# Optimization experiments

Measured on AMD Instinct MI355X. Metric: run time of the kernel, lower is better.

The kernel has to match this reference:

```python
import jax, jax.numpy as jnp
import numpy as np

KW = 4.0                     # kernel_width
P = int(np.ceil(KW) + 2)     # taps per axis = 6


def _axis_indices_offsets(in_s, out_s):
    """Replicates get_indice for one axis (1-based math, then 0-based clip)."""
    x = jnp.arange(1, out_s + 1, dtype=jnp.float32)
    scale = float(out_s) / float(in_s)
    u = x / scale + 0.5 * (1.0 - 1.0 / scale)
    left = jnp.floor(u - KW / 2)
    idx = left[:, None] + jnp.arange(P, dtype=jnp.float32)[None, :]   # [out, P]
    off = u[:, None] - idx                                            # offsets BEFORE clipping
    idx = jnp.clip(idx, 1.0, float(in_s)).astype(jnp.int32) - 1       # 0-based, clipped
    return idx, off, scale


def _cubic(x):
    a = jnp.abs(x)
    a2 = x * x
    a3 = a * a2
    return jnp.where(a <= 1.0, 1.5 * a3 - 2.5 * a2 + 1.0,
                     jnp.where(a <= 2.0, -0.5 * a3 + 2.5 * a2 - 4.0 * a + 2.0, 0.0))


def setup_inputs() -> dict:
    key = jax.random.key(0)
    inp = jax.random.normal(key, (4, 3, 768, 768), dtype=jnp.float32)
    return {"input": inp, "out_h": 384, "out_w": 384}


def reference(input, out_h, out_w):
    B, C, H, W = input.shape
    idx0, off0, sh = _axis_indices_offsets(H, out_h)   # idx0,[oh,P]; off0,[oh,P]
    idx1, off1, sw = _axis_indices_offsets(W, out_w)

    # normal_bicubic=True branch: offsets scaled by (oh/H, ow/W), rotation = identity
    wh = _cubic(off0 * sh)                             # [oh, P]
    ww = _cubic(off1 * sw)                             # [ow, P]
    wmat = wh[:, None, :, None] * ww[None, :, None, :] # [oh, ow, P, P]
    wmat = wmat / jnp.sum(wmat, axis=(-1, -2), keepdims=True)

    # gather: [B, C, oh, ow, P, P] via separable advanced indexing
    gathered = input[:, :, idx0[:, None, :, None], idx1[None, :, None, :]]

    res = jnp.einsum('bcijpq,ijpq->bcij', gathered, wmat)  # [B, C, oh, ow]
    kernel = jnp.broadcast_to(wmat.reshape(1, 1, out_h, out_w, P * P),
                              (B, 1, out_h, out_w, P * P))
    return res, kernel
```

## Files before the change

### kernel.cpp

```cpp
#include <hip/hip_runtime.h>

#define BB 4
#define CC 3
#define IH 768
#define IW 768
#define OH 384
#define OW 384
#define PP 6

#define RES_N   (BB * CC * OH * OW)
#define KER_N   (BB * OH * OW * PP * PP)

__device__ __forceinline__ float cubic_w(float x) {
    float a  = fabsf(x);
    float a2 = a * a;
    float a3 = a2 * a;
    if (a <= 1.0f) return 1.5f * a3 - 2.5f * a2 + 1.0f;
    if (a <= 2.0f) return -0.5f * a3 + 2.5f * a2 - 4.0f * a + 2.0f;
    return 0.0f;
}

__device__ __forceinline__ void axis_weights(int o, float scale, float inv_scale,
                                             int in_s, int* idx, float* w) {
    float x = (float)(o + 1);
    float u = x * inv_scale + 0.5f * (1.0f - inv_scale);
    float left = floorf(u - 2.0f);
    float sum = 0.0f;
    #pragma unroll
    for (int p = 0; p < PP; ++p) {
        float idxf = left + (float)p;
        float off  = u - idxf;
        float cl   = fminf(fmaxf(idxf, 1.0f), (float)in_s);
        idx[p] = (int)cl - 1;
        w[p] = cubic_w(off * scale);
        sum += w[p];
    }
    float inv = 1.0f / sum;
    #pragma unroll
    for (int p = 0; p < PP; ++p) w[p] *= inv;
}

__global__ __launch_bounds__(256) void bicubic_res_kernel(
        const float* __restrict__ in, float* __restrict__ out) {
    int t = blockIdx.x * blockDim.x + threadIdx.x;
    if (t >= RES_N) return;
    int j   = t % OW;
    int rem = t / OW;
    int i   = rem % OH;
    int bc  = rem / OH;

    int   ri[PP], ci[PP];
    float wh[PP], ww[PP];
    axis_weights(i, 0.5f, 2.0f, IH, ri, wh);
    axis_weights(j, 0.5f, 2.0f, IW, ci, ww);

    const float* base = in + (size_t)bc * (IH * IW);
    float acc = 0.0f;
    #pragma unroll
    for (int p = 0; p < PP; ++p) {
        const float* row = base + (size_t)ri[p] * IW;
        float rsum = 0.0f;
        #pragma unroll
        for (int q = 0; q < PP; ++q)
            rsum = fmaf(ww[q], row[ci[q]], rsum);
        acc = fmaf(wh[p], rsum, acc);
    }
    out[t] = acc;
}

__global__ __launch_bounds__(256) void bicubic_wmat_kernel(float* __restrict__ kout) {
    int b = blockIdx.x / OH;
    int i = blockIdx.x % OH;

    __shared__ float s_ww[OW * PP];
    __shared__ float s_wh[PP];

    for (int j = threadIdx.x; j < OW; j += blockDim.x) {
        int   ci[PP];
        float w[PP];
        axis_weights(j, 0.5f, 2.0f, IW, ci, w);
        #pragma unroll
        for (int q = 0; q < PP; ++q) s_ww[j * PP + q] = w[q];
    }
    if (threadIdx.x == 0) {
        int   ri[PP];
        float w[PP];
        axis_weights(i, 0.5f, 2.0f, IH, ri, w);
        #pragma unroll
        for (int p = 0; p < PP; ++p) s_wh[p] = w[p];
    }
    __syncthreads();

    float4* dst = (float4*)(kout + (size_t)(b * OH + i) * (OW * PP * PP));
    const int NF4 = OW * PP * PP / 4;
    for (int f = threadIdx.x; f < NF4; f += blockDim.x) {
        int e = f * 4;
        int j = e / 36;
        int k = e % 36;
        float v[4];
        #pragma unroll
        for (int tt = 0; tt < 4; ++tt) {
            int kk = k + tt;
            int p = kk / PP;
            int q = kk - p * PP;
            v[tt] = s_wh[p] * s_ww[j * PP + q];
        }
        float4 o;
        o.x = v[0]; o.y = v[1]; o.z = v[2]; o.w = v[3];
        dst[f] = o;
    }
}

extern "C" void kernel_launch(void* const* d_in, const int* in_sizes, int n_in,
                              void* d_out, int out_size, void* d_ws, size_t ws_size,
                              hipStream_t stream) {
    const float* input = (const float*)d_in[0];
    float* out = (float*)d_out;
    float* res  = out;
    float* kout = out + RES_N;

    {
        int blocks = (RES_N + 255) / 256;
        bicubic_res_kernel<<<blocks, 256, 0, stream>>>(input, res);
    }
    {
        int blocks = BB * OH;
        bicubic_wmat_kernel<<<blocks, 256, 0, stream>>>(kout);
    }
}
```

Before: 146.2 us.

## Fuse resample and weight kernels using constant 2x-downsample weights and register tiling

Replaces the two kernels with one fused launch. Because the scale is exactly 0.5, every output pixel has the same six normalized taps, so the weights are computed once as constants and the per-pixel index/weight math is dropped. Each thread computes a 2x4 output tile from an 8x16 input window loaded as float4s, reusing horizontal partial sums across the two output rows. The weight tensor output becomes a repeating 9-float4 pattern written by grid-stride stores. This relies on the fixed 768->384 shape, and the clamped edge handling has to match the reference's clipped indices.

```diff
diff --git a/kernel.cpp b/kernel.cpp
--- a/kernel.cpp
+++ b/kernel.cpp
@@ -1,113 +1,128 @@
 #include <hip/hip_runtime.h>
 
-#define BB 4
-#define CC 3
-#define IH 768
-#define IW 768
-#define OH 384
-#define OW 384
-#define PP 6
 
-#define RES_N   (BB * CC * OH * OW)
-#define KER_N   (BB * OH * OW * PP * PP)
+#define IHW 768
+#define OHW 384
+#define PP  6
+#define NBC 12
+#define RES_N  (NBC * OHW * OHW)
+#define KER_N  (4 * OHW * OHW * PP * PP)
+#define KER_F4 (KER_N / 4)
+
+#define SX_N 96
+#define SY_N 192
+#define RES_THREADS (NBC * SX_N * SY_N)
+#define RES_BLOCKS  (RES_THREADS / 256)
+#define WMAT_THREADS 147456
+#define WMAT_BLOCKS  (WMAT_THREADS / 256)
 
 __device__ __forceinline__ float cubic_w(float x) {
     float a  = fabsf(x);
-    float a2 = a * a;
-    float a3 = a2 * a;
-    if (a <= 1.0f) return 1.5f * a3 - 2.5f * a2 + 1.0f;
-    if (a <= 2.0f) return -0.5f * a3 + 2.5f * a2 - 4.0f * a + 2.0f;
-    return 0.0f;
+    float a2 = a * a, a3 = a2 * a;
+    float r1 = 1.5f * a3 - 2.5f * a2 + 1.0f;
+    float r2 = -0.5f * a3 + 2.5f * a2 - 4.0f * a + 2.0f;
+    return a <= 1.0f ? r1 : (a <= 2.0f ? r2 : 0.0f);
 }
 
-__device__ __forceinline__ void axis_weights(int o, float scale, float inv_scale,
-                                             int in_s, int* idx, float* w) {
-    float x = (float)(o + 1);
-    float u = x * inv_scale + 0.5f * (1.0f - inv_scale);
-    float left = floorf(u - 2.0f);
-    float sum = 0.0f;
+__device__ __forceinline__ void calc_wn(float wn[PP]) {
+    float s = 0.0f;
     #pragma unroll
-    for (int p = 0; p < PP; ++p) {
-        float idxf = left + (float)p;
-        float off  = u - idxf;
-        float cl   = fminf(fmaxf(idxf, 1.0f), (float)in_s);
-        idx[p] = (int)cl - 1;
-        w[p] = cubic_w(off * scale);
-        sum += w[p];
+    for (int q = 0; q < PP; ++q) {
+        wn[q] = cubic_w((2.5f - (float)q) * 0.5f);
+        s += wn[q];
     }
-    float inv = 1.0f / sum;
+    float inv = 1.0f / s;
     #pragma unroll
-    for (int p = 0; p < PP; ++p) w[p] *= inv;
+    for (int q = 0; q < PP; ++q) wn[q] *= inv;
 }
 
-__global__ __launch_bounds__(256) void bicubic_res_kernel(
+__global__ __launch_bounds__(256) void bicubic_fused_kernel(
         const float* __restrict__ in, float* __restrict__ out) {
-    int t = blockIdx.x * blockDim.x + threadIdx.x;
-    if (t >= RES_N) return;
-    int j   = t % OW;
-    int rem = t / OW;
-    int i   = rem % OH;
-    int bc  = rem / OH;
+    float* res  = out;
+    float* kout = out + RES_N;
 
-    int   ri[PP], ci[PP];
-    float wh[PP], ww[PP];
-    axis_weights(i, 0.5f, 2.0f, IH, ri, wh);
-    axis_weights(j, 0.5f, 2.0f, IW, ci, ww);
+    float wn[PP];
+    calc_wn(wn);
 
-    const float* base = in + (size_t)bc * (IH * IW);
-    float acc = 0.0f;
-    #pragma unroll
-    for (int p = 0; p < PP; ++p) {
-        const float* row = base + (size_t)ri[p] * IW;
-        float rsum = 0.0f;
+    int blk = blockIdx.x;
+    if (blk < RES_BLOCKS) {
+        int g   = blk * 256 + threadIdx.x;
+        int sx  = g % SX_N;
+        int t1  = g / SX_N;
+        int sy  = t1 % SY_N;
+        int bc  = t1 / SY_N;
+        int j0  = 4 * sx;
+        int i0  = 2 * sy;
+        int col0 = 8 * sx - 4;
+        const float* base = in + (size_t)bc * (IHW * IHW);
+        bool edge = (sx == 0) | (sx == SX_N - 1);
+
+        float acc[2][4] = {{0.f,0.f,0.f,0.f},{0.f,0.f,0.f,0.f}};
+
         #pragma unroll
-        for (int q = 0; q < PP; ++q)
-            rsum = fmaf(ww[q], row[ci[q]], rsum);
-        acc = fmaf(wh[p], rsum, acc);
-    }
-    out[t] = acc;
-}
+        for (int k = 0; k < 8; ++k) {
+            int row = 4 * sy - 2 + k;
+            row = min(max(row, 0), IHW - 1);
+            const float* rp = base + (size_t)row * IHW;
 
-__global__ __launch_bounds__(256) void bicubic_wmat_kernel(float* __restrict__ kout) {
-    int b = blockIdx.x / OH;
-    int i = blockIdx.x % OH;
+            float v[16];
+            if (edge) {
+                #pragma unroll
+                for (int m = 0; m < 16; ++m) {
+                    int c = col0 + m;
+                    c = min(max(c, 0), IHW - 1);
+                    v[m] = rp[c];
+                }
+            } else {
+                const float4* p4 = (const float4*)(rp + col0);
+                float4 A = p4[0], B = p4[1], C = p4[2], D = p4[3];
+                v[0]=A.x; v[1]=A.y; v[2]=A.z; v[3]=A.w;
+                v[4]=B.x; v[5]=B.y; v[6]=B.z; v[7]=B.w;
+                v[8]=C.x; v[9]=C.y; v[10]=C.z; v[11]=C.w;
+                v[12]=D.x; v[13]=D.y; v[14]=D.z; v[15]=D.w;
+            }
 
-    __shared__ float s_ww[OW * PP];
-    __shared__ float s_wh[PP];
+            #pragma unroll
+            for (int c = 0; c < 4; ++c) {
+                float h = wn[0] * v[2*c + 2];
+                h = fmaf(wn[1], v[2*c + 3], h);
+                h = fmaf(wn[2], v[2*c + 4], h);
+                h = fmaf(wn[3], v[2*c + 5], h);
+                h = fmaf(wn[4], v[2*c + 6], h);
+                h = fmaf(wn[5], v[2*c + 7], h);
+                #pragma unroll
+                for (int o = 0; o < 2; ++o) {
+                    int p = k - 2 * o;
+                    if (p >= 0 && p < PP)
+                        acc[o][c] = fmaf(wn[p], h, acc[o][c]);
+                }
+            }
+        }
 
-    for (int j = threadIdx.x; j < OW; j += blockDim.x) {
-        int   ci[PP];
-        float w[PP];
-        axis_weights(j, 0.5f, 2.0f, IW, ci, w);
         #pragma unroll
-        for (int q = 0; q < PP; ++q) s_ww[j * PP + q] = w[q];
-    }
-    if (threadIdx.x == 0) {
-        int   ri[PP];
-        float w[PP];
-        axis_weights(i, 0.5f, 2.0f, IH, ri, w);
-        #pragma unroll
-        for (int p = 0; p < PP; ++p) s_wh[p] = w[p];
-    }
-    __syncthreads();
-
-    float4* dst = (float4*)(kout + (size_t)(b * OH + i) * (OW * PP * PP));
-    const int NF4 = OW * PP * PP / 4;
-    for (int f = threadIdx.x; f < NF4; f += blockDim.x) {
-        int e = f * 4;
-        int j = e / 36;
-        int k = e % 36;
-        float v[4];
-        #pragma unroll
-        for (int tt = 0; tt < 4; ++tt) {
-            int kk = k + tt;
-            int p = kk / PP;
-            int q = kk - p * PP;
-            v[tt] = s_wh[p] * s_ww[j * PP + q];
+        for (int o = 0; o < 2; ++o) {
+            float4 r;
+            r.x = acc[o][0]; r.y = acc[o][1]; r.z = acc[o][2]; r.w = acc[o][3];
+            *(float4*)(res + ((size_t)(bc * OHW + i0 + o) * OHW + j0)) = r;
         }
-        float4 o;
-        o.x = v[0]; o.y = v[1]; o.z = v[2]; o.w = v[3];
-        dst[f] = o;
+    } else {
+        int t = (blk - RES_BLOCKS) * 256 + threadIdx.x;
+        int r = t % 9;
+        float4 pat;
+        switch (r) {
+            case 0: pat = make_float4(wn[0]*wn[0], wn[0]*wn[1], wn[0]*wn[2], wn[0]*wn[3]); break;
+            case 1: pat = make_float4(wn[0]*wn[4], wn[0]*wn[5], wn[1]*wn[0], wn[1]*wn[1]); break;
+            case 2: pat = make_float4(wn[1]*wn[2], wn[1]*wn[3], wn[1]*wn[4], wn[1]*wn[5]); break;
+            case 3: pat = make_float4(wn[2]*wn[0], wn[2]*wn[1], wn[2]*wn[2], wn[2]*wn[3]); break;
+            case 4: pat = make_float4(wn[2]*wn[4], wn[2]*wn[5], wn[3]*wn[0], wn[3]*wn[1]); break;
+            case 5: pat = make_float4(wn[3]*wn[2], wn[3]*wn[3], wn[3]*wn[4], wn[3]*wn[5]); break;
+            case 6: pat = make_float4(wn[4]*wn[0], wn[4]*wn[1], wn[4]*wn[2], wn[4]*wn[3]); break;
+            case 7: pat = make_float4(wn[4]*wn[4], wn[4]*wn[5], wn[5]*wn[0], wn[5]*wn[1]); break;
+            default: pat = make_float4(wn[5]*wn[2], wn[5]*wn[3], wn[5]*wn[4], wn[5]*wn[5]); break;
+        }
+        float4* k4 = (float4*)kout;
+        for (int f = t; f < KER_F4; f += WMAT_THREADS)
+            k4[f] = pat;
     }
 }
 
@@ -116,15 +131,5 @@
                               hipStream_t stream) {
     const float* input = (const float*)d_in[0];
     float* out = (float*)d_out;
-    float* res  = out;
-    float* kout = out + RES_N;
-
-    {
-        int blocks = (RES_N + 255) / 256;
-        bicubic_res_kernel<<<blocks, 256, 0, stream>>>(input, res);
-    }
-    {
-        int blocks = BB * OH;
-        bicubic_wmat_kernel<<<blocks, 256, 0, stream>>>(kout);
-    }
+    bicubic_fused_kernel<<<RES_BLOCKS + WMAT_BLOCKS, 256, 0, stream>>>(input, out);
 }
```

After: 119.2 us. 1.23x faster.
